# Performance work log

Hardware: AMD Instinct MI355X
Metric: run time of the kernel (lower is better)

The kernel has to match this reference:

```python
import jax, jax.numpy as jnp
import numpy as np

STRIDE, PAD, DIL = 1, 1, 1
EPS = 1e-12
RHO_LIM = 1.0 - 1e-6
PI = jnp.pi


def clamp_pg(x, lo=0.0):
    # clamp value but pass gradient through (clamp_preserve_grad)
    return x + jax.lax.stop_gradient(jnp.maximum(x, lo) - x)


def setup_inputs() -> dict:
    key = jax.random.key(0)
    B, N, T, K = 8, 128, 1024, 3
    k = jax.random.uniform(key, (B, B, N, T, 2), dtype=jnp.float32)
    leak = jnp.array(1.0, dtype=jnp.float32)
    alpha = jnp.full((1, 1, K), 1.0 / K, dtype=jnp.float32)
    beta = jnp.array(0.0, dtype=jnp.float32)
    return {"k": k, "leak": leak, "alpha": alpha, "beta": beta}


def reference(k, leak, alpha, beta):
    k_gp, k_ntk = k[..., 0], k[..., 1]          # (B,B,N,T) each
    B, _, N, T = k_gp.shape

    # v[b,t] = k_gp[b,b,0,t]  (diagonal over batch dims, first lag)
    ar = jnp.arange(B)
    v = k_gp[ar, ar, 0, :]                      # (B,T)
    v_pad = jnp.pad(v, ((0, 0), (0, N - 1)))    # (B, T+N-1)

    v_xx = v[:, None, None, :]                  # (B,1,1,T)
    idx = jnp.arange(N)[:, None] + jnp.arange(T)[None, :]  # (N,T)
    v_yy = v_pad[:, idx][None]                  # (1,B,N,T): v_pad[b, n+t]

    # calculate_statistics
    std_x = jnp.sqrt(jnp.maximum(v_xx, 0.0))
    std_y = jnp.sqrt(jnp.maximum(v_yy, 0.0))
    denom = jnp.maximum(std_x * std_y, EPS)
    rho = jnp.clip(k_gp / denom, -RHO_LIM, RHO_LIM)  # (B,B,N,T)

    a = clamp_pg(leak)
    theta = jnp.arccos(rho)
    s = jnp.sqrt(1.0 - rho * rho)
    one_m = (1.0 - a) ** 2
    coef = 1.0 + a * a
    # leaky-ReLU arccos kernel and its derivative kernel
    c0 = std_x * std_y / (2.0 * PI) * (one_m * s + rho * (coef * PI - one_m * theta))
    c1 = (coef * PI - one_m * theta) / (2.0 * PI)

    w = clamp_pg(alpha)                         # (1,1,K)

    def conv(x):  # x: (B,B,N,T) -> (B,B,N,T')
        y = jax.lax.conv_general_dilated(
            x.reshape(-1, 1, T), w, window_strides=(STRIDE,),
            padding=[(PAD, PAD)], rhs_dilation=(DIL,),
            dimension_numbers=("NCH", "OIH", "NCH"))
        return y.reshape(B, B, N, -1)

    kg = conv(c0)
    kn = conv(c1 * k_ntk) + kg

    b = clamp_pg(beta)
    kg = kg + b
    kn = kn + b
    return jnp.stack([kg, kn], axis=-1)
```

## Files before the change

kernel.cpp:

```cpp
#include <hip/hip_runtime.h>
#include <math.h>

#define BDIM 8
#define NDIM 128
#define TDIM 1024
#define TPB 1024
#define CT 128
#define NCHUNK (TDIM / CT)
#define WPB (TPB / 64)
#define NIT (NDIM / WPB)
#define SXN (CT + 2)
#define SYN (NDIM + CT + 1)

#define EPS_F 1e-12f
#define RHO_LIM_F (1.0f - 1e-6f)
#define PI_F 3.14159265358979323846f

__device__ __forceinline__ void kfun(float kgp, float kntk, float sx, float sy,
                                     float one_m, float coef, bool fast,
                                     float& c0, float& cn)
{
    const float inv2pi = 0.15915494309189535f;
    const float p = sx * sy;
    if (fast) {
        const float hc = 0.5f * coef;
        const float pr = p * RHO_LIM_F;
        c0 = hc * fminf(fmaxf(kgp, -pr), pr);
        cn = hc * kntk;
    } else {
        const float r  = fminf(fmaxf(kgp * __builtin_amdgcn_rcpf(fmaxf(p, EPS_F)), -RHO_LIM_F), RHO_LIM_F);
        const float th = acosf(r);
        const float s  = sqrtf(1.0f - r * r);
        const float br = coef * PI_F - one_m * th;
        c0 = p * inv2pi * (one_m * s + r * br);
        cn = br * inv2pi * kntk;
    }
}

__global__ __launch_bounds__(TPB) void conv_arccos_kernel(
    const float* __restrict__ k,
    const float* __restrict__ leak,
    const float* __restrict__ alpha,
    const float* __restrict__ beta,
    float* __restrict__ out)
{
    __shared__ float sx_lds[SXN];
    __shared__ float sy_lds[SYN];

    const int chunk = blockIdx.x & (NCHUNK - 1);
    const int bb    = blockIdx.x >> 3;
    const int b2    = bb & (BDIM - 1);
    const int b1    = bb >> 3;
    const int tc    = chunk * CT;

    const int tid  = threadIdx.x;
    const int lane = tid & 63;
    const int wid  = tid >> 6;

    const float a   = fmaxf(leak[0], 0.0f);
    const float w0  = fmaxf(alpha[0], 0.0f);
    const float w1  = fmaxf(alpha[1], 0.0f);
    const float w2  = fmaxf(alpha[2], 0.0f);
    const float bia = fmaxf(beta[0], 0.0f);

    const float one_m = (1.0f - a) * (1.0f - a);
    const float coef  = 1.0f + a * a;
    const bool  fast  = (one_m == 0.0f);

    const float2* vrx = (const float2*)k + (size_t)(b1 * BDIM + b1) * NDIM * TDIM;
    const float2* vry = (const float2*)k + (size_t)(b2 * BDIM + b2) * NDIM * TDIM;

    if (tid < SXN) {
        const int t = tc - 1 + tid;
        const float v = (t >= 0 && t < TDIM) ? vrx[t].x : 0.0f;
        sx_lds[tid] = sqrtf(fmaxf(v, 0.0f));
    } else if (tid < SXN + SYN) {
        const int j = tid - SXN;
        const int e = tc - 1 + j;
        const float v = (e >= 0 && e < TDIM) ? vry[e].x : 0.0f;
        sy_lds[j] = sqrtf(fmaxf(v, 0.0f));
    }
    __syncthreads();

    const float sx0 = sx_lds[2 * lane + 1];
    const float sx1 = sx_lds[2 * lane + 2];
    const float sxm = sx_lds[0];
    const float sxp = sx_lds[CT + 1];

    const bool lhalo = (lane == 0)  && (tc > 0);
    const bool rhalo = (lane == 63) && (tc + CT < TDIM);
    const int  g     = (tc >> 1) + lane;

    #pragma unroll 2
    for (int i = 0; i < NIT; ++i) {
        const int n   = i * WPB + wid;
        const int row = bb * NDIM + n;
        const float* krow = k + (size_t)row * (TDIM * 2);

        const float4 kv = ((const float4*)krow)[g];
        const float sy0 = sy_lds[n + 2 * lane + 1];
        const float sy1 = sy_lds[n + 2 * lane + 2];

        float c00, cn0, c01, cn1;
        kfun(kv.x, kv.y, sx0, sy0, one_m, coef, fast, c00, cn0);
        kfun(kv.z, kv.w, sx1, sy1, one_m, coef, fast, c01, cn1);

        float c0lh = 0.0f, cnlh = 0.0f, c0rh = 0.0f, cnrh = 0.0f;
        if (lhalo) {
            const float2 kl = ((const float2*)krow)[tc - 1];
            kfun(kl.x, kl.y, sxm, sy_lds[n], one_m, coef, fast, c0lh, cnlh);
        }
        if (rhalo) {
            const float2 kr = ((const float2*)krow)[tc + CT];
            kfun(kr.x, kr.y, sxp, sy_lds[n + CT + 1], one_m, coef, fast, c0rh, cnrh);
        }

        float c0l = __shfl_up(c01, 1);
        float cnl = __shfl_up(cn1, 1);
        float c0r = __shfl_down(c00, 1);
        float cnr = __shfl_down(cn0, 1);
        if (lane == 0)  { c0l = c0lh; cnl = cnlh; }
        if (lane == 63) { c0r = c0rh; cnr = cnrh; }

        const float kg0 = fmaf(w0, c0l, fmaf(w1, c00, fmaf(w2, c01, bia)));
        const float kg1 = fmaf(w0, c00, fmaf(w1, c01, fmaf(w2, c0r, bia)));
        const float kn0 = fmaf(w0, cnl, fmaf(w1, cn0, fmaf(w2, cn1, kg0)));
        const float kn1 = fmaf(w0, cn0, fmaf(w1, cn1, fmaf(w2, cnr, kg1)));

        ((float4*)(out + (size_t)row * (TDIM * 2)))[g] = make_float4(kg0, kn0, kg1, kn1);
    }
}

extern "C" void kernel_launch(void* const* d_in, const int* in_sizes, int n_in,
                              void* d_out, int out_size, void* d_ws, size_t ws_size,
                              hipStream_t stream) {
    const float* k     = (const float*)d_in[0];
    const float* leak  = (const float*)d_in[1];
    const float* alpha = (const float*)d_in[2];
    const float* beta  = (const float*)d_in[3];
    float* out = (float*)d_out;

    const int n_blocks = BDIM * BDIM * NCHUNK;
    conv_arccos_kernel<<<n_blocks, TPB, 0, stream>>>(k, leak, alpha, beta, out);
}
```

Baseline: 122.1 us.

## Batch all row loads up front and split N across smaller blocks

Each block now covers half of the N rows with 512 threads, and the grid doubles. Every thread issues all 8 float4 row loads and the halo loads before doing any compute, so more memory requests are in flight at once. The halo handling now runs one uniform kfun per row instead of separate left and right branches. The cost is higher register pressure from holding 8 rows of data at a time, which the occupancy hint of 4 blocks per CU may not accommodate.

```diff
diff --git a/kernel.cpp b/kernel.cpp
--- a/kernel.cpp
+++ b/kernel.cpp
@@ -4,13 +4,15 @@
 #define BDIM 8
 #define NDIM 128
 #define TDIM 1024
-#define TPB 1024
+#define TPB 512
 #define CT 128
 #define NCHUNK (TDIM / CT)
 #define WPB (TPB / 64)
-#define NIT (NDIM / WPB)
+#define NIT 8
+#define RPB (WPB * NIT)
+#define NHALF (NDIM / RPB)
 #define SXN (CT + 2)
-#define SYN (NDIM + CT + 1)
+#define SYN (RPB + CT + 1)
 
 #define EPS_F 1e-12f
 #define RHO_LIM_F (1.0f - 1e-6f)
@@ -37,7 +39,7 @@
     }
 }
 
-__global__ __launch_bounds__(TPB) void conv_arccos_kernel(
+__global__ __launch_bounds__(TPB, 4) void conv_arccos_kernel(
     const float* __restrict__ k,
     const float* __restrict__ leak,
     const float* __restrict__ alpha,
@@ -48,10 +50,12 @@
     __shared__ float sy_lds[SYN];
 
     const int chunk = blockIdx.x & (NCHUNK - 1);
-    const int bb    = blockIdx.x >> 3;
+    const int nh    = (blockIdx.x >> 3) & (NHALF - 1);
+    const int bb    = blockIdx.x >> 4;
     const int b2    = bb & (BDIM - 1);
     const int b1    = bb >> 3;
     const int tc    = chunk * CT;
+    const int nbase = nh * RPB;
 
     const int tid  = threadIdx.x;
     const int lane = tid & 63;
@@ -76,7 +80,7 @@
         sx_lds[tid] = sqrtf(fmaxf(v, 0.0f));
     } else if (tid < SXN + SYN) {
         const int j = tid - SXN;
-        const int e = tc - 1 + j;
+        const int e = nbase + tc - 1 + j;
         const float v = (e >= 0 && e < TDIM) ? vry[e].x : 0.0f;
         sy_lds[j] = sqrtf(fmaxf(v, 0.0f));
     }
@@ -84,50 +88,62 @@
 
     const float sx0 = sx_lds[2 * lane + 1];
     const float sx1 = sx_lds[2 * lane + 2];
-    const float sxm = sx_lds[0];
-    const float sxp = sx_lds[CT + 1];
+    const bool hval = (lane == 0) ? (tc > 0)
+                    : ((lane == 63) ? (tc + CT < TDIM) : false);
+    const float sxh = hval ? ((lane == 0) ? sx_lds[0] : sx_lds[CT + 1]) : 0.0f;
+    const int   eh  = (lane == 0) ? (tc - 1) : (tc + CT);
+    const int   jh  = (lane == 63) ? (CT + 1) : 0;
+    const int   g   = (tc >> 1) + lane;
 
-    const bool lhalo = (lane == 0)  && (tc > 0);
-    const bool rhalo = (lane == 63) && (tc + CT < TDIM);
-    const int  g     = (tc >> 1) + lane;
+    const size_t rowstride = (size_t)TDIM * 2;
+    const float* krow0 = k   + ((size_t)(bb * NDIM + nbase)) * rowstride;
+    float*       orow0 = out + ((size_t)(bb * NDIM + nbase)) * rowstride;
 
-    #pragma unroll 2
+    float4 kv[NIT];
+    #pragma unroll
     for (int i = 0; i < NIT; ++i) {
-        const int n   = i * WPB + wid;
-        const int row = bb * NDIM + n;
-        const float* krow = k + (size_t)row * (TDIM * 2);
+        const float* kr = krow0 + (size_t)(i * WPB + wid) * rowstride;
+        kv[i] = ((const float4*)kr)[g];
+    }
+    float khg[NIT], khn[NIT];
+    #pragma unroll
+    for (int i = 0; i < NIT; ++i) {
+        khg[i] = 0.0f; khn[i] = 0.0f;
+        if (hval) {
+            const float2 h = ((const float2*)(krow0 + (size_t)(i * WPB + wid) * rowstride))[eh];
+            khg[i] = h.x; khn[i] = h.y;
+        }
+    }
+    float sy0[NIT], sy1[NIT], syh[NIT];
+    #pragma unroll
+    for (int i = 0; i < NIT; ++i) {
+        const int nl = i * WPB + wid;
+        sy0[i] = sy_lds[nl + 2 * lane + 1];
+        sy1[i] = sy_lds[nl + 2 * lane + 2];
+        syh[i] = sy_lds[nl + jh];
+    }
 
-        const float4 kv = ((const float4*)krow)[g];
-        const float sy0 = sy_lds[n + 2 * lane + 1];
-        const float sy1 = sy_lds[n + 2 * lane + 2];
-
-        float c00, cn0, c01, cn1;
-        kfun(kv.x, kv.y, sx0, sy0, one_m, coef, fast, c00, cn0);
-        kfun(kv.z, kv.w, sx1, sy1, one_m, coef, fast, c01, cn1);
-
-        float c0lh = 0.0f, cnlh = 0.0f, c0rh = 0.0f, cnrh = 0.0f;
-        if (lhalo) {
-            const float2 kl = ((const float2*)krow)[tc - 1];
-            kfun(kl.x, kl.y, sxm, sy_lds[n], one_m, coef, fast, c0lh, cnlh);
-        }
-        if (rhalo) {
-            const float2 kr = ((const float2*)krow)[tc + CT];
-            kfun(kr.x, kr.y, sxp, sy_lds[n + CT + 1], one_m, coef, fast, c0rh, cnrh);
-        }
+    #pragma unroll
+    for (int i = 0; i < NIT; ++i) {
+        float c00, cn0, c01, cn1, c0h, cnh;
+        kfun(kv[i].x, kv[i].y, sx0, sy0[i], one_m, coef, fast, c00, cn0);
+        kfun(kv[i].z, kv[i].w, sx1, sy1[i], one_m, coef, fast, c01, cn1);
+        kfun(khg[i],  khn[i],  sxh, syh[i], one_m, coef, fast, c0h, cnh);
 
         float c0l = __shfl_up(c01, 1);
         float cnl = __shfl_up(cn1, 1);
         float c0r = __shfl_down(c00, 1);
         float cnr = __shfl_down(cn0, 1);
-        if (lane == 0)  { c0l = c0lh; cnl = cnlh; }
-        if (lane == 63) { c0r = c0rh; cnr = cnrh; }
+        if (lane == 0)  { c0l = c0h; cnl = cnh; }
+        if (lane == 63) { c0r = c0h; cnr = cnh; }
 
         const float kg0 = fmaf(w0, c0l, fmaf(w1, c00, fmaf(w2, c01, bia)));
         const float kg1 = fmaf(w0, c00, fmaf(w1, c01, fmaf(w2, c0r, bia)));
         const float kn0 = fmaf(w0, cnl, fmaf(w1, cn0, fmaf(w2, cn1, kg0)));
         const float kn1 = fmaf(w0, cn0, fmaf(w1, cn1, fmaf(w2, cnr, kg1)));
 
-        ((float4*)(out + (size_t)row * (TDIM * 2)))[g] = make_float4(kg0, kn0, kg1, kn1);
+        ((float4*)(orow0 + (size_t)(i * WPB + wid) * rowstride))[g] =
+            make_float4(kg0, kn0, kg1, kn1);
     }
 }
 
@@ -140,6 +156,6 @@
     const float* beta  = (const float*)d_in[3];
     float* out = (float*)d_out;
 
-    const int n_blocks = BDIM * BDIM * NCHUNK;
+    const int n_blocks = BDIM * BDIM * NHALF * NCHUNK;
     conv_arccos_kernel<<<n_blocks, TPB, 0, stream>>>(k, leak, alpha, beta, out);
 }
```

Result: no change. 120.1 us (-1.7%).
